# Kernel optimization log

Measured on AMD Instinct MI355X. Metric: run time of the kernel, lower is better.

The kernel has to match this reference:

```python
import jax, jax.numpy as jnp
import numpy as np
from jax import lax

B, L, D_MODEL = 4, 512, 256
N_LAYERS = 6
EXPAND = 2
D_INNER = EXPAND * D_MODEL  # 512
D_STATE = 16
D_CONV = 4
DT_RANK = (D_MODEL + 15) // 16  # 16
EPS = 1e-5


def silu(x):
    return x * jax.nn.sigmoid(x)


def rmsnorm(x, w):
    var = jnp.mean(x * x, axis=-1, keepdims=True)
    return x * lax.rsqrt(var + EPS) * w


def setup_inputs() -> dict:
    key = jax.random.key(0)
    ks = jax.random.split(key, 12)
    s = lambda *sh: 0.02
    inp = {
        "x": jax.random.normal(ks[0], (B, L, D_MODEL), dtype=jnp.float32),
        "norm_w": jnp.ones((N_LAYERS, D_MODEL), jnp.float32),
        "W_in": jax.random.normal(ks[1], (N_LAYERS, 2 * D_INNER, D_MODEL), jnp.float32) * 0.02,
        "b_in": jnp.zeros((N_LAYERS, 2 * D_INNER), jnp.float32),
        "conv_w": jax.random.normal(ks[2], (N_LAYERS, D_INNER, D_CONV), jnp.float32) * 0.2,
        "W_x": jax.random.normal(ks[3], (N_LAYERS, DT_RANK + 2 * D_STATE, D_INNER), jnp.float32) * 0.02,
        "dt_w": jax.random.normal(ks[4], (N_LAYERS, D_INNER, DT_RANK), jnp.float32) * 0.1,
        "dt_b": jax.random.uniform(ks[5], (N_LAYERS, D_INNER), jnp.float32, -4.0, -2.0),
        "A_log": jnp.log(jnp.broadcast_to(jnp.arange(1, D_STATE + 1, dtype=jnp.float32), (N_LAYERS, D_INNER, D_STATE))),
        "D": jnp.ones((N_LAYERS, D_INNER), jnp.float32),
        "W_out": jax.random.normal(ks[6], (N_LAYERS, D_MODEL, D_INNER), jnp.float32) * 0.02,
        "b_out": jnp.zeros((N_LAYERS, D_MODEL), jnp.float32),
    }
    return inp


def mamba_block(x, W_in, b_in, conv_w, W_x, dt_w, dt_b, A_log, D, W_out, b_out):
    # input projection -> (B, L, 2*d_inner)
    xz = jnp.einsum("bld,ed->ble", x, W_in) + b_in
    xin, z = xz[..., :D_INNER], xz[..., D_INNER:]
    # depthwise causal conv over time (groups = d_inner, left pad d_conv-1)
    xc = lax.conv_general_dilated(
        xin.transpose(0, 2, 1),            # (B, C, L)
        conv_w[:, None, :],                # (C, 1, K)
        window_strides=(1,),
        padding=[(D_CONV - 1, 0)],
        feature_group_count=D_INNER,
        dimension_numbers=("NCH", "OIH", "NCH"),
    ).transpose(0, 2, 1)
    u = silu(xc)                           # (B, L, d_inner)
    # data-dependent dt, B, C
    xdbc = jnp.einsum("bld,rd->blr", u, W_x)
    dt = xdbc[..., :DT_RANK]
    Bm = xdbc[..., DT_RANK:DT_RANK + D_STATE]
    Cm = xdbc[..., DT_RANK + D_STATE:]
    delta = jax.nn.softplus(jnp.einsum("blr,dr->bld", dt, dt_w) + dt_b)
    A = -jnp.exp(A_log)                    # (d_inner, d_state)
    dA = jnp.exp(jnp.einsum("bld,dn->bldn", delta, A))
    dBu = jnp.einsum("bld,bln->bldn", delta * u, Bm)
    # selective scan over time
    def step(h, inp):
        dA_t, dBu_t, C_t = inp
        h = dA_t * h + dBu_t               # (B, d_inner, d_state)
        y_t = jnp.einsum("bdn,bn->bd", h, C_t)
        return h, y_t
    h0 = jnp.zeros((B, D_INNER, D_STATE), x.dtype)
    _, ys = lax.scan(step, h0, (dA.transpose(1, 0, 2, 3), dBu.transpose(1, 0, 2, 3), Cm.transpose(1, 0, 2)))
    y = ys.transpose(1, 0, 2) + u * D      # skip connection D*u
    y = y * silu(z)
    return jnp.einsum("bld,md->blm", y, W_out) + b_out


def reference(x, norm_w, W_in, b_in, conv_w, W_x, dt_w, dt_b, A_log, D, W_out, b_out):
    for i in range(N_LAYERS):
        x = x + mamba_block(rmsnorm(x, norm_w[i]), W_in[i], b_in[i], conv_w[i], W_x[i], dt_w[i], dt_b[i], A_log[i], D[i], W_out[i], b_out[i])
    return x
```

## Files before the change

### kernel.cpp

```cpp
#include <hip/hip_runtime.h>
#include <hip/hip_bf16.h>

#define B_SZ 4
#define L_SZ 512
#define D_MODEL 256
#define D_INNER 512
#define D_STATE 16
#define DT_RANK 16
#define N_LAYERS 6
#define BL (B_SZ * L_SZ)

typedef __bf16 bf16_t;
typedef __bf16 bf16x8 __attribute__((ext_vector_type(8)));
typedef __bf16 bf16x4 __attribute__((ext_vector_type(4)));
typedef float  f32x4  __attribute__((ext_vector_type(4)));

__device__ __forceinline__ float row_allreduce16(float x)
{
    int v;
    v = __builtin_amdgcn_mov_dpp(__float_as_int(x), 0x121, 0xf, 0xf, true);
    x += __int_as_float(v);
    v = __builtin_amdgcn_mov_dpp(__float_as_int(x), 0x122, 0xf, 0xf, true);
    x += __int_as_float(v);
    v = __builtin_amdgcn_mov_dpp(__float_as_int(x), 0x124, 0xf, 0xf, true);
    x += __int_as_float(v);
    v = __builtin_amdgcn_mov_dpp(__float_as_int(x), 0x128, 0xf, 0xf, true);
    x += __int_as_float(v);
    return x;
}

__global__ __launch_bounds__(256) void cast3_kernel(
    const float* __restrict__ s0, const float* __restrict__ s1,
    const float* __restrict__ s2, bf16_t* __restrict__ dst,
    int n0, int n1, int n2)
{
    int i = blockIdx.x * 256 + threadIdx.x;
    const float* s; int off;
    if (i < n0)            { s = s0; off = i; }
    else if (i < n0 + n1)  { s = s1; off = i - n0; }
    else if (i < n0+n1+n2) { s = s2; off = i - n0 - n1; }
    else return;
    const float4 v = *(const float4*)(s + (size_t)off * 4);
    bf16x4 o;
    o[0] = (bf16_t)v.x; o[1] = (bf16_t)v.y;
    o[2] = (bf16_t)v.z; o[3] = (bf16_t)v.w;
    *(bf16x4*)(dst + (size_t)i * 4) = o;
}

__global__ __launch_bounds__(256) void rmsnorm_kernel(
    const float* __restrict__ x, const float* __restrict__ w,
    bf16_t* __restrict__ o)
{
    int row  = blockIdx.x * 4 + (threadIdx.x >> 6);
    int lane = threadIdx.x & 63;
    const float4 v = *(const float4*)(x + (size_t)row * D_MODEL + lane * 4);
    float ss = v.x * v.x + v.y * v.y + v.z * v.z + v.w * v.w;
    #pragma unroll
    for (int off = 32; off; off >>= 1) ss += __shfl_xor(ss, off);
    float rs = rsqrtf(ss * (1.f / D_MODEL) + 1e-5f);
    const float4 wv = *(const float4*)(w + lane * 4);
    bf16x4 ov;
    ov[0] = (bf16_t)(v.x * rs * wv.x);
    ov[1] = (bf16_t)(v.y * rs * wv.y);
    ov[2] = (bf16_t)(v.z * rs * wv.z);
    ov[3] = (bf16_t)(v.w * rs * wv.w);
    *(bf16x4*)(o + (size_t)row * D_MODEL + lane * 4) = ov;
}

__global__ __launch_bounds__(256) void win_kernel(
    const bf16_t* __restrict__ A,
    const bf16_t* __restrict__ Bw,
    const float* __restrict__ bias,
    float* __restrict__ C,
    float* __restrict__ Z)
{
    constexpr int K = 256, BK = 64;
    __shared__ bf16_t As[64][K + 8];
    __shared__ bf16_t Bs[64][BK + 8];

    const int tid  = threadIdx.x;
    const int wave = tid >> 6, lane = tid & 63;
    const int wm = wave >> 1, wn = wave & 1;
    const int lm = lane & 15, quad = lane >> 4;
    const int m0 = blockIdx.y * 64, n0 = blockIdx.x * 64;

    #pragma unroll
    for (int i = tid; i < 64 * (K / 8); i += 256) {
        int r = i >> 5, c8 = i & 31;
        *(bf16x8*)&As[r][c8 * 8] =
            *(const bf16x8*)(A + (size_t)(m0 + r) * K + c8 * 8);
    }

    f32x4 acc[2][2] = {};
    for (int k0 = 0; k0 < K; k0 += BK) {
        #pragma unroll
        for (int i = tid; i < 64 * (BK / 8); i += 256) {
            int r = i >> 3, c8 = i & 7;
            *(bf16x8*)&Bs[r][c8 * 8] =
                *(const bf16x8*)(Bw + (size_t)(n0 + r) * K + k0 + c8 * 8);
        }
        __syncthreads();
        #pragma unroll
        for (int ks = 0; ks < 2; ++ks) {
            bf16x8 af[2], bfr[2];
            #pragma unroll
            for (int i = 0; i < 2; ++i)
                af[i] = *(const bf16x8*)&As[wm * 32 + i * 16 + lm][k0 + ks * 32 + quad * 8];
            #pragma unroll
            for (int j = 0; j < 2; ++j)
                bfr[j] = *(const bf16x8*)&Bs[wn * 32 + j * 16 + lm][ks * 32 + quad * 8];
            #pragma unroll
            for (int i = 0; i < 2; ++i)
                #pragma unroll
                for (int j = 0; j < 2; ++j)
                    acc[i][j] = __builtin_amdgcn_mfma_f32_16x16x32_bf16(
                        af[i], bfr[j], acc[i][j], 0, 0, 0);
        }
        __syncthreads();
    }

    if (n0 >= D_INNER) {
        #pragma unroll
        for (int i = 0; i < 2; ++i) {
            int rowbase = m0 + wm * 32 + i * 16 + quad * 4;
            #pragma unroll
            for (int j = 0; j < 2; ++j) {
                int col = n0 + wn * 32 + j * 16 + lm;
                float4 o;
                #pragma unroll
                for (int r = 0; r < 4; ++r) {
                    float v = acc[i][j][r] + bias[col];
                    ((float*)&o)[r] = v / (1.f + __expf(-v));
                }
                *(float4*)(Z + (size_t)(col - D_INNER) * BL + rowbase) = o;
            }
        }
        return;
    }

    #pragma unroll
    for (int i = 0; i < 2; ++i) {
        #pragma unroll
        for (int j = 0; j < 2; ++j) {
            int col = n0 + wn * 32 + j * 16 + lm;
            #pragma unroll
            for (int r = 0; r < 4; ++r) {
                int rowm = m0 + wm * 32 + i * 16 + quad * 4 + r;
                C[(size_t)rowm * D_INNER + col] = acc[i][j][r] + bias[col];
            }
        }
    }
}

template<int WM, int WN, int TM_T, int TN_T>
__global__ __launch_bounds__(64 * WM * WN) void gemm_wout(
    const bf16_t* __restrict__ A, int lda,
    const bf16_t* __restrict__ Bw, int ldb,
    const float* __restrict__ bias,
    const float* __restrict__ R, int ldr,
    float* __restrict__ C, int ldc, int K)
{
    constexpr int BK = 64;
    constexpr int BM = WM * TM_T * 16;
    constexpr int BN = WN * TN_T * 16;
    constexpr int NT = 64 * WM * WN;
    constexpr int LDK = BK + 8;
    __shared__ bf16_t As[BM][LDK];
    __shared__ bf16_t Bs[BN][LDK];

    const int tid  = threadIdx.x;
    const int wave = tid >> 6, lane = tid & 63;
    const int wm = wave / WN, wn = wave % WN;
    const int lm = lane & 15, quad = lane >> 4;
    const int m0 = blockIdx.y * BM, n0 = blockIdx.x * BN;

    f32x4 acc[TM_T][TN_T] = {};

    for (int k0 = 0; k0 < K; k0 += BK) {
        #pragma unroll
        for (int i = tid; i < BM * (BK / 8); i += NT) {
            int r = i >> 3, c8 = i & 7;
            *(bf16x8*)&As[r][c8 * 8] =
                *(const bf16x8*)(A + (size_t)(m0 + r) * lda + k0 + c8 * 8);
        }
        #pragma unroll
        for (int i = tid; i < BN * (BK / 8); i += NT) {
            int r = i >> 3, c8 = i & 7;
            *(bf16x8*)&Bs[r][c8 * 8] =
                *(const bf16x8*)(Bw + (size_t)(n0 + r) * ldb + k0 + c8 * 8);
        }
        __syncthreads();
        #pragma unroll
        for (int ks = 0; ks < BK / 32; ++ks) {
            bf16x8 af[TM_T], bfr[TN_T];
            #pragma unroll
            for (int i = 0; i < TM_T; ++i)
                af[i] = *(const bf16x8*)&As[wm * TM_T * 16 + i * 16 + lm][ks * 32 + quad * 8];
            #pragma unroll
            for (int j = 0; j < TN_T; ++j)
                bfr[j] = *(const bf16x8*)&Bs[wn * TN_T * 16 + j * 16 + lm][ks * 32 + quad * 8];
            #pragma unroll
            for (int i = 0; i < TM_T; ++i)
                #pragma unroll
                for (int j = 0; j < TN_T; ++j)
                    acc[i][j] = __builtin_amdgcn_mfma_f32_16x16x32_bf16(
                        af[i], bfr[j], acc[i][j], 0, 0, 0);
        }
        __syncthreads();
    }

    #pragma unroll
    for (int i = 0; i < TM_T; ++i) {
        #pragma unroll
        for (int j = 0; j < TN_T; ++j) {
            int col = n0 + wn * TN_T * 16 + j * 16 + lm;
            #pragma unroll
            for (int r = 0; r < 4; ++r) {
                int rowm = m0 + wm * TM_T * 16 + i * 16 + quad * 4 + r;
                C[(size_t)rowm * ldc + col] =
                    acc[i][j][r] + bias[col] + R[(size_t)rowm * ldr + col];
            }
        }
    }
}

__global__ __launch_bounds__(256) void wx_conv_kernel(
    const float* __restrict__ xzx,
    const float* __restrict__ cw,
    const bf16_t* __restrict__ Bw,
    float* __restrict__ uT,
    float* __restrict__ xdbcT)
{
    constexpr int K = 512;
    __shared__ float  xs[19][516];
    __shared__ bf16_t us[16][520];
    __shared__ f32x4  part[4][3][64];

    const int tid  = threadIdx.x;
    const int wave = tid >> 6, lane = tid & 63;
    const int lm = lane & 15, quad = lane >> 4;
    const int m0 = blockIdx.x * 16;

    for (int q = tid; q < 19 * 128; q += 256) {
        int rx = q >> 7, c4 = (q & 127) * 4;
        int mr = m0 - 3 + rx;
        float4 v = make_float4(0.f, 0.f, 0.f, 0.f);
        if (mr >= 0) v = *(const float4*)(xzx + (size_t)mr * K + c4);
        *(float4*)&xs[rx][c4] = v;
    }
    __syncthreads();

    #pragma unroll
    for (int it = 0; it < 8; ++it) {
        int item = tid + it * 256;
        int d = item >> 2, rg = item & 3;
        const float4 wv = *(const float4*)(cw + d * 4);
        float4 o;
        #pragma unroll
        for (int e = 0; e < 4; ++e) {
            int ro = rg * 4 + e;
            int t  = (m0 + ro) & (L_SZ - 1);
            float a = wv.w * xs[ro + 3][d];
            if (t >= 1) a += wv.z * xs[ro + 2][d];
            if (t >= 2) a += wv.y * xs[ro + 1][d];
            if (t >= 3) a += wv.x * xs[ro + 0][d];
            a = a / (1.f + __expf(-a));
            ((float*)&o)[e] = a;
            us[ro][d] = (bf16_t)a;
        }
        *(float4*)(uT + (size_t)d * BL + m0 + rg * 4) = o;
    }
    __syncthreads();

    f32x4 acc[3] = {};
    const int kb = wave * 128 + quad * 8;
    #pragma unroll
    for (int ks = 0; ks < 4; ++ks) {
        int k0 = kb + ks * 32;
        bf16x8 af = *(const bf16x8*)&us[lm][k0];
        #pragma unroll
        for (int j = 0; j < 3; ++j) {
            bf16x8 bfr = *(const bf16x8*)(Bw + (size_t)(j * 16 + lm) * K + k0);
            acc[j] = __builtin_amdgcn_mfma_f32_16x16x32_bf16(af, bfr, acc[j], 0, 0, 0);
        }
    }
    #pragma unroll
    for (int j = 0; j < 3; ++j) part[wave][j][lane] = acc[j];
    __syncthreads();

    if (tid < 192) {
        int j = tid >> 6, l = tid & 63;
        f32x4 s = part[0][j][l];
        s += part[1][j][l];
        s += part[2][j][l];
        s += part[3][j][l];
        int col = j * 16 + (l & 15);
        float4 v = make_float4(s[0], s[1], s[2], s[3]);
        *(float4*)(xdbcT + (size_t)col * BL + m0 + (l >> 4) * 4) = v;
    }
}

__global__ __launch_bounds__(1024, 4) void scan_kernel(
    const float* __restrict__ xdbcT,
    const float* __restrict__ uT,
    const float* __restrict__ szT,
    const float* __restrict__ dt_w,
    const float* __restrict__ dt_b,
    const float* __restrict__ A_log,
    const float* __restrict__ Dv,
    bf16_t* __restrict__ y)
{
    constexpr int TC = 32;
    constexpr int NW = L_SZ / TC;

    int blk  = blockIdx.x;
    int b    = blk >> 7;
    int dg   = blk & 127;
    int wave = threadIdx.x >> 6;
    int lane = threadIdx.x & 63;
    int d    = dg * 4 + (lane >> 4);
    int n    = lane & 15;

    __shared__ float lds_Ap[NW][64];
    __shared__ float lds_he[NW][64];

    float Adn = -__expf(A_log[d * D_STATE + n]);
    float Dd  = Dv[d];
    int r0 = b * L_SZ + wave * TC;

    const float* Brow = xdbcT  + (size_t)(DT_RANK + n) * BL;
    const float* Crow = xdbcT  + (size_t)(DT_RANK + D_STATE + n) * BL;
    const float* urow = uT     + (size_t)d * BL;
    const float* zrow = szT    + (size_t)d * BL;

    float myd[2];
    {
        float w16[16];
        #pragma unroll
        for (int k4 = 0; k4 < 4; ++k4) {
            float4 wv = *(const float4*)(dt_w + (size_t)d * 16 + k4 * 4);
            w16[k4*4+0] = wv.x; w16[k4*4+1] = wv.y;
            w16[k4*4+2] = wv.z; w16[k4*4+3] = wv.w;
        }
        float bdt = dt_b[d];
        #pragma unroll
        for (int g = 0; g < 2; ++g) {
            int t = r0 + g * 16 + n;
            float a = bdt;
            #pragma unroll
            for (int k = 0; k < 16; ++k)
                a += xdbcT[(size_t)k * BL + t] * w16[k];
            myd[g] = (a > 20.f) ? a : __logf(1.f + __expf(a));
        }
    }
    const int sbase = lane & 48;

    float hl[TC], Pl[TC];
    float h = 0.f, P = 1.f;
    #pragma unroll
    for (int g = 0; g < 2; ++g) {
        #pragma unroll
        for (int j4 = 0; j4 < 4; ++j4) {
            int rb = r0 + g * 16 + j4 * 4;
            f32x4 Bv = *(const f32x4*)(Brow + rb);
            f32x4 uv = *(const f32x4*)(urow + rb);
            float dA[4], dBu[4];
            #pragma unroll
            for (int k = 0; k < 4; ++k) {
                float dlj = __shfl(myd[g], sbase | (j4 * 4 + k));
                dA[k]  = __expf(dlj * Adn);
                dBu[k] = dlj * uv[k] * Bv[k];
            }
            #pragma unroll
            for (int k = 0; k < 4; ++k) {
                int t = g * 16 + j4 * 4 + k;
                h = dA[k] * h + dBu[k];
                P *= dA[k];
                hl[t] = h;
                Pl[t] = P;
            }
        }
    }
    lds_Ap[wave][lane] = P;
    lds_he[wave][lane] = h;
    __syncthreads();

    float H = 0.f;
    for (int j = 0; j < wave; ++j)
        H = lds_Ap[j][lane] * H + lds_he[j][lane];

    #pragma unroll
    for (int t0 = 0; t0 < TC; t0 += 16) {
        float py[16];
        #pragma unroll
        for (int j4 = 0; j4 < 4; ++j4) {
            int rb = r0 + t0 + j4 * 4;
            f32x4 Cc = *(const f32x4*)(Crow + rb);
            #pragma unroll
            for (int k = 0; k < 4; ++k) {
                int t = t0 + j4 * 4 + k;
                py[j4*4+k] = (hl[t] + Pl[t] * H) * Cc[k];
            }
        }
        #pragma unroll
        for (int j = 0; j < 16; ++j)
            py[j] = row_allreduce16(py[j]);
        if (n == 0) {
            #pragma unroll
            for (int j4 = 0; j4 < 4; ++j4) {
                int rb = r0 + t0 + j4 * 4;
                f32x4 uv = *(const f32x4*)(urow + rb);
                f32x4 sz = *(const f32x4*)(zrow + rb);
                #pragma unroll
                for (int k = 0; k < 4; ++k) {
                    int row = rb + k;
                    y[(size_t)row * D_INNER + d] =
                        (bf16_t)((py[j4*4+k] + uv[k] * Dd) * sz[k]);
                }
            }
        }
    }
}

extern "C" void kernel_launch(void* const* d_in, const int* in_sizes, int n_in,
                              void* d_out, int out_size, void* d_ws, size_t ws_size,
                              hipStream_t stream)
{
    const float* x_in   = (const float*)d_in[0];
    const float* norm_w = (const float*)d_in[1];
    const float* W_in   = (const float*)d_in[2];
    const float* b_in   = (const float*)d_in[3];
    const float* conv_w = (const float*)d_in[4];
    const float* W_x    = (const float*)d_in[5];
    const float* dt_w   = (const float*)d_in[6];
    const float* dt_b   = (const float*)d_in[7];
    const float* A_log  = (const float*)d_in[8];
    const float* Dv     = (const float*)d_in[9];
    const float* W_out  = (const float*)d_in[10];
    const float* b_out  = (const float*)d_in[11];
    float* out = (float*)d_out;

    float* ws     = (float*)d_ws;
    float* xz     = ws;
    float* uT     = xz     + BL * D_INNER;
    float* szT    = uT     + D_INNER * BL;
    float* xdbcT  = szT    + D_INNER * BL;
    bf16_t* bws   = (bf16_t*)(xdbcT + 48 * BL);
    bf16_t* xn_bf = bws;
    bf16_t* y_bf  = xn_bf + BL * D_MODEL;
    bf16_t* Wi_bf = y_bf  + BL * D_INNER;
    bf16_t* Wx_bf = Wi_bf + N_LAYERS * 2 * D_INNER * D_MODEL;
    bf16_t* Wo_bf = Wx_bf + N_LAYERS * 48 * D_INNER;

    {
        int n0 = N_LAYERS * 2 * D_INNER * D_MODEL / 4;
        int n1 = N_LAYERS * 48 * D_INNER / 4;
        int n2 = N_LAYERS * D_MODEL * D_INNER / 4;
        cast3_kernel<<<(n0 + n1 + n2 + 255) / 256, 256, 0, stream>>>(
            W_in, W_x, W_out, Wi_bf, n0, n1, n2);
    }

    for (int i = 0; i < N_LAYERS; ++i) {
        const float* xcur = (i == 0) ? x_in : out;

        rmsnorm_kernel<<<BL / 4, 256, 0, stream>>>(xcur, norm_w + i * D_MODEL, xn_bf);

        win_kernel<<<dim3(1024 / 64, 2048 / 64), 256, 0, stream>>>(
            xn_bf, Wi_bf + (size_t)i * 2 * D_INNER * D_MODEL,
            b_in + i * 2 * D_INNER, xz, szT);

        wx_conv_kernel<<<BL / 16, 256, 0, stream>>>(
            xz, conv_w + i * D_INNER * 4,
            Wx_bf + (size_t)i * 48 * D_INNER, uT, xdbcT);

        scan_kernel<<<512, 1024, 0, stream>>>(
            xdbcT, uT, szT,
            dt_w + (size_t)i * D_INNER * DT_RANK, dt_b + i * D_INNER,
            A_log + (size_t)i * D_INNER * D_STATE, Dv + i * D_INNER, y_bf);

        gemm_wout<2, 2, 2, 2><<<dim3(256 / 64, 2048 / 64), 256, 0, stream>>>(
            y_bf, D_INNER, Wo_bf + (size_t)i * D_MODEL * D_INNER, D_INNER,
            b_out + i * D_MODEL, xcur, D_MODEL, out, D_MODEL, D_INNER);
    }
}
```

Baseline: 483.0 us.

## Split wx_conv over two K halves with partial sums; shrink Wout tile

The conv+W_x kernel now splits the inner dimension into two halves, one per block, which doubles the grid. Each half writes its own partial xdbc result to a separate buffer. The scan kernel reads both partial buffers and adds them when it loads dt, B and C. The output GEMM also switches to a smaller M tile with twice as many blocks. Together these aim to raise occupancy on the small grids, at the cost of extra global reads in the scan and extra workspace.

```diff
diff --git a/kernel.cpp b/kernel.cpp
--- a/kernel.cpp
+++ b/kernel.cpp
@@ -229,58 +229,61 @@
     const float* __restrict__ cw,
     const bf16_t* __restrict__ Bw,
     float* __restrict__ uT,
-    float* __restrict__ xdbcT)
-{
-    constexpr int K = 512;
-    __shared__ float  xs[19][516];
-    __shared__ bf16_t us[16][520];
+    float* __restrict__ xdbcP)
+{
+    constexpr int K  = 512;
+    constexpr int KH = 256;
+    __shared__ float  xs[19][KH + 4];
+    __shared__ bf16_t us[16][KH + 8];
     __shared__ f32x4  part[4][3][64];
 
     const int tid  = threadIdx.x;
     const int wave = tid >> 6, lane = tid & 63;
     const int lm = lane & 15, quad = lane >> 4;
-    const int m0 = blockIdx.x * 16;
-
-    for (int q = tid; q < 19 * 128; q += 256) {
-        int rx = q >> 7, c4 = (q & 127) * 4;
+    const int blk = blockIdx.x;
+    const int kh  = blk & 1;
+    const int m0  = (blk >> 1) * 16;
+    const int d0  = kh * KH;
+
+    for (int q = tid; q < 19 * (KH / 4); q += 256) {
+        int rx = q >> 6, c4 = (q & 63) * 4;
         int mr = m0 - 3 + rx;
         float4 v = make_float4(0.f, 0.f, 0.f, 0.f);
-        if (mr >= 0) v = *(const float4*)(xzx + (size_t)mr * K + c4);
+        if (mr >= 0) v = *(const float4*)(xzx + (size_t)mr * K + d0 + c4);
         *(float4*)&xs[rx][c4] = v;
     }
     __syncthreads();
 
     #pragma unroll
-    for (int it = 0; it < 8; ++it) {
+    for (int it = 0; it < 4; ++it) {
         int item = tid + it * 256;
-        int d = item >> 2, rg = item & 3;
-        const float4 wv = *(const float4*)(cw + d * 4);
+        int dl = item >> 2, rg = item & 3;
+        const float4 wv = *(const float4*)(cw + (d0 + dl) * 4);
         float4 o;
         #pragma unroll
         for (int e = 0; e < 4; ++e) {
             int ro = rg * 4 + e;
             int t  = (m0 + ro) & (L_SZ - 1);
-            float a = wv.w * xs[ro + 3][d];
-            if (t >= 1) a += wv.z * xs[ro + 2][d];
-            if (t >= 2) a += wv.y * xs[ro + 1][d];
-            if (t >= 3) a += wv.x * xs[ro + 0][d];
+            float a = wv.w * xs[ro + 3][dl];
+            if (t >= 1) a += wv.z * xs[ro + 2][dl];
+            if (t >= 2) a += wv.y * xs[ro + 1][dl];
+            if (t >= 3) a += wv.x * xs[ro + 0][dl];
             a = a / (1.f + __expf(-a));
             ((float*)&o)[e] = a;
-            us[ro][d] = (bf16_t)a;
-        }
-        *(float4*)(uT + (size_t)d * BL + m0 + rg * 4) = o;
+            us[ro][dl] = (bf16_t)a;
+        }
+        *(float4*)(uT + (size_t)(d0 + dl) * BL + m0 + rg * 4) = o;
     }
     __syncthreads();
 
     f32x4 acc[3] = {};
-    const int kb = wave * 128 + quad * 8;
-    #pragma unroll
-    for (int ks = 0; ks < 4; ++ks) {
-        int k0 = kb + ks * 32;
+    #pragma unroll
+    for (int ks = 0; ks < 2; ++ks) {
+        int k0 = wave * 64 + ks * 32 + quad * 8;
         bf16x8 af = *(const bf16x8*)&us[lm][k0];
         #pragma unroll
         for (int j = 0; j < 3; ++j) {
-            bf16x8 bfr = *(const bf16x8*)(Bw + (size_t)(j * 16 + lm) * K + k0);
+            bf16x8 bfr = *(const bf16x8*)(Bw + (size_t)(j * 16 + lm) * K + d0 + k0);
             acc[j] = __builtin_amdgcn_mfma_f32_16x16x32_bf16(af, bfr, acc[j], 0, 0, 0);
         }
     }
@@ -296,12 +299,12 @@
         s += part[3][j][l];
         int col = j * 16 + (l & 15);
         float4 v = make_float4(s[0], s[1], s[2], s[3]);
-        *(float4*)(xdbcT + (size_t)col * BL + m0 + (l >> 4) * 4) = v;
+        *(float4*)(xdbcP + (size_t)kh * 48 * BL + (size_t)col * BL + m0 + (l >> 4) * 4) = v;
     }
 }
 
 __global__ __launch_bounds__(1024, 4) void scan_kernel(
-    const float* __restrict__ xdbcT,
+    const float* __restrict__ xdbcP,
     const float* __restrict__ uT,
     const float* __restrict__ szT,
     const float* __restrict__ dt_w,
@@ -312,6 +315,7 @@
 {
     constexpr int TC = 32;
     constexpr int NW = L_SZ / TC;
+    constexpr int PSTR = 48 * BL;
 
     int blk  = blockIdx.x;
     int b    = blk >> 7;
@@ -328,10 +332,10 @@
     float Dd  = Dv[d];
     int r0 = b * L_SZ + wave * TC;
 
-    const float* Brow = xdbcT  + (size_t)(DT_RANK + n) * BL;
-    const float* Crow = xdbcT  + (size_t)(DT_RANK + D_STATE + n) * BL;
-    const float* urow = uT     + (size_t)d * BL;
-    const float* zrow = szT    + (size_t)d * BL;
+    const float* Brow  = xdbcP + (size_t)(DT_RANK + n) * BL;
+    const float* Crow  = xdbcP + (size_t)(DT_RANK + D_STATE + n) * BL;
+    const float* urow  = uT    + (size_t)d * BL;
+    const float* zrow  = szT   + (size_t)d * BL;
 
     float myd[2];
     {
@@ -349,7 +353,7 @@
             float a = bdt;
             #pragma unroll
             for (int k = 0; k < 16; ++k)
-                a += xdbcT[(size_t)k * BL + t] * w16[k];
+                a += (xdbcP[(size_t)k * BL + t] + xdbcP[(size_t)k * BL + PSTR + t]) * w16[k];
             myd[g] = (a > 20.f) ? a : __logf(1.f + __expf(a));
         }
     }
@@ -363,6 +367,8 @@
         for (int j4 = 0; j4 < 4; ++j4) {
             int rb = r0 + g * 16 + j4 * 4;
             f32x4 Bv = *(const f32x4*)(Brow + rb);
+            f32x4 Bv1 = *(const f32x4*)(Brow + PSTR + rb);
+            Bv += Bv1;
             f32x4 uv = *(const f32x4*)(urow + rb);
             float dA[4], dBu[4];
             #pragma unroll
@@ -396,6 +402,8 @@
         for (int j4 = 0; j4 < 4; ++j4) {
             int rb = r0 + t0 + j4 * 4;
             f32x4 Cc = *(const f32x4*)(Crow + rb);
+            f32x4 Cc1 = *(const f32x4*)(Crow + PSTR + rb);
+            Cc += Cc1;
             #pragma unroll
             for (int k = 0; k < 4; ++k) {
                 int t = t0 + j4 * 4 + k;
@@ -444,8 +452,8 @@
     float* xz     = ws;
     float* uT     = xz     + BL * D_INNER;
     float* szT    = uT     + D_INNER * BL;
-    float* xdbcT  = szT    + D_INNER * BL;
-    bf16_t* bws   = (bf16_t*)(xdbcT + 48 * BL);
+    float* xdbcP  = szT    + D_INNER * BL;
+    bf16_t* bws   = (bf16_t*)(xdbcP + 2 * 48 * BL);
     bf16_t* xn_bf = bws;
     bf16_t* y_bf  = xn_bf + BL * D_MODEL;
     bf16_t* Wi_bf = y_bf  + BL * D_INNER;
@@ -469,16 +477,16 @@
             xn_bf, Wi_bf + (size_t)i * 2 * D_INNER * D_MODEL,
             b_in + i * 2 * D_INNER, xz, szT);
 
-        wx_conv_kernel<<<BL / 16, 256, 0, stream>>>(
+        wx_conv_kernel<<<(BL / 16) * 2, 256, 0, stream>>>(
             xz, conv_w + i * D_INNER * 4,
-            Wx_bf + (size_t)i * 48 * D_INNER, uT, xdbcT);
+            Wx_bf + (size_t)i * 48 * D_INNER, uT, xdbcP);
 
         scan_kernel<<<512, 1024, 0, stream>>>(
-            xdbcT, uT, szT,
+            xdbcP, uT, szT,
             dt_w + (size_t)i * D_INNER * DT_RANK, dt_b + i * D_INNER,
             A_log + (size_t)i * D_INNER * D_STATE, Dv + i * D_INNER, y_bf);
 
-        gemm_wout<2, 2, 2, 2><<<dim3(256 / 64, 2048 / 64), 256, 0, stream>>>(
+        gemm_wout<2, 2, 1, 2><<<dim3(256 / 64, 2048 / 32), 256, 0, stream>>>(
             y_bf, D_INNER, Wo_bf + (size_t)i * D_MODEL * D_INNER, D_INNER,
             b_out + i * D_MODEL, xcur, D_MODEL, out, D_MODEL, D_INNER);
     }
```

New measurement: 539.9 us. +11.8%, slower.
